# Performance work log

Measured on AMD Instinct MI355X. Metric: run time of the kernel, lower is better.

Reference implementation:

```python
import jax, jax.numpy as jnp
from jax import lax
import numpy as np

# hyperparams (from init_kwargs)
NB_CLASSES = 100
SZ_EMBED = 128
SCALE = 3.0
LAM = 0.7          # np.random.beta(1,1) draw, fixed for determinism
OT_EPS = 0.05
SINK_THRESH = 0.1
SINK_MAX_ITER = 100
DN = ('NCHW', 'OIHW', 'NCHW')


def l2norm(x, axis):
    # F.normalize: x / max(||x||, 1e-12)
    n = jnp.sqrt(jnp.sum(x * x, axis=axis, keepdims=True))
    return x / jnp.maximum(n, 1e-12)


def encode(x, W_enc, W_feat):
    c = jax.nn.relu(lax.conv_general_dilated(x, W_enc, (2, 2), 'SAME', dimension_numbers=DN))
    f = jax.nn.relu(lax.conv_general_dilated(c, W_feat, (1, 1), 'SAME', dimension_numbers=DN))
    feat = f.mean(axis=(2, 3))  # (B, SZ_EMBED)
    return c, feat


def decode(c, W_dec):
    return lax.conv_transpose(c, W_dec, (2, 2), 'SAME', dimension_numbers=DN)


def sinkhorn(K, u, v):
    # faithful to torch loop: update r, c; break when mean|r-r0| < thresh
    def cond(s):
        i, r, c, err = s
        return jnp.logical_and(i < SINK_MAX_ITER, err >= SINK_THRESH)

    def body(s):
        i, r, c, _ = s
        r0 = r
        r = u / jnp.einsum('bij,bj->bi', K, c)
        c = v / jnp.einsum('bji,bj->bi', K, r)
        err = jnp.mean(jnp.abs(r - r0))
        return (i + 1, r, c, err)

    init = (jnp.int32(0), jnp.ones_like(u), jnp.ones_like(v), jnp.array(jnp.inf, K.dtype))
    _, r, c, _ = lax.while_loop(cond, body, init)
    return r[:, :, None] * c[:, None, :] * K  # (B, S, S)


def pair_wise_wdist(x, y):
    B, C, H, W = x.shape
    S = H * W
    xf = l2norm(x.reshape(B, C, S), axis=1)  # unit vectors per spatial location
    yf = l2norm(y.reshape(B, C, S), axis=1)
    sim = jnp.einsum('bcs,bcm->bsm', xf, yf)  # (B, S, S)
    # ||x-y||^2 = 2 - 2*sim for unit vectors (avoids (B,C,S,S) intermediate)
    dist1 = jnp.sqrt(jnp.maximum(2.0 - 2.0 * sim, 0.0) + 1e-6)
    u = jnp.full((B, S), 1.0 / S, dtype=sim.dtype)
    v = jnp.full((B, S), 1.0 / S, dtype=sim.dtype)
    K = lax.stop_gradient(jnp.exp(-(1.0 - sim) / OT_EPS))  # torch.no_grad
    T = lax.stop_gradient(sinkhorn(K, u, v))
    dist = jnp.sum(T * dist1, axis=(1, 2))
    return dist, T


def metric_loss(X, labels, P):
    Pn = SCALE * l2norm(P, axis=-1)
    Xn = SCALE * l2norm(X, axis=-1)
    # squared pairwise distance X vs P
    D = (jnp.sum(Xn * Xn, -1)[:, None] + jnp.sum(Pn * Pn, -1)[None, :]
         - 2.0 * Xn @ Pn.T)
    logp = jax.nn.log_softmax(-D, axis=-1)
    # smoothing_const=0 -> one-hot labels
    return -jnp.mean(logp[jnp.arange(X.shape[0]), labels])


def reference(xa, xb, la, lb, proxies, W_enc, W_feat, W_dec):
    B, C, H, W = xa.shape
    c_xa, feat_xa = encode(xa, W_enc, W_feat)
    xa_hat = decode(c_xa, W_dec)
    c_xb, feat_xb = encode(xb, W_enc, W_feat)
    xb_hat = decode(c_xb, W_dec)

    struct_dist, T = pair_wise_wdist(xa, xb)

    xa_fl = l2norm(xa, axis=1).reshape(B, C, -1)
    xb_fl = l2norm(xb, axis=1).reshape(B, C, -1)
    # faithful to the original einsum (k and j summed independently)
    xb_tomix = jnp.einsum('bmk,bji->bmi', xa_fl, T)
    xa_tomix = jnp.einsum('bmk,bji->bmi', xb_fl, jnp.swapaxes(T, 1, 2))

    lam = LAM
    mixed_xa = (lam * xa.reshape(B, C, -1) + (1 - lam) * xa_tomix).reshape(B, C, H, W)
    mixed_xb = (lam * xb.reshape(B, C, -1) + (1 - lam) * xb_tomix).reshape(B, C, H, W)

    l_x_rec_a = jnp.mean(jnp.square(xa_hat - xa))
    l_x_rec_b = jnp.mean(jnp.square(xb_hat - xb))

    feat_ma = mixed_xa.mean(axis=(2, 3))  # adaptive_avg_pool2d -> (B, C)
    feat_mb = mixed_xb.mean(axis=(2, 3))

    l_c_rec_a = metric_loss(feat_xa, la, proxies)
    l_c_rec_b = metric_loss(feat_xb, lb, proxies)
    l_c_rec_ma = lam * metric_loss(feat_ma, la, proxies) + (1 - lam) * metric_loss(feat_ma, lb, proxies)
    l_c_rec_mb = lam * metric_loss(feat_mb, lb, proxies) + (1 - lam) * metric_loss(feat_mb, la, proxies)

    l_total = l_x_rec_a + l_x_rec_b + l_c_rec_a + l_c_rec_b + l_c_rec_ma + l_c_rec_mb
    return jnp.stack([l_total, l_x_rec_a, l_x_rec_b, l_c_rec_a, l_c_rec_b, l_c_rec_ma, l_c_rec_mb])


def setup_inputs() -> dict:
    key = jax.random.key(0)
    ks = jax.random.split(key, 8)
    B, C, H, W = 32, 128, 32, 32
    xa = jax.random.normal(ks[0], (B, C, H, W), jnp.float32)
    xb = jax.random.normal(ks[1], (B, C, H, W), jnp.float32)
    la = jax.random.randint(ks[2], (B,), 0, NB_CLASSES)
    lb = jax.random.randint(ks[3], (B,), 0, NB_CLASSES)
    proxies = jax.random.normal(ks[4], (NB_CLASSES, SZ_EMBED), jnp.float32) / 8.0
    W_enc = jax.random.normal(ks[5], (2 * C, C, 3, 3), jnp.float32) * 0.02
    W_feat = jax.random.normal(ks[6], (SZ_EMBED, 2 * C, 3, 3), jnp.float32) * 0.02
    W_dec = jax.random.normal(ks[7], (C, 2 * C, 3, 3), jnp.float32) * 0.02
    return {"xa": xa, "xb": xb, "la": la, "lb": lb, "proxies": proxies,
            "W_enc": W_enc, "W_feat": W_feat, "W_dec": W_dec}
```

## Files before the change

### kernel.cpp

```cpp
#include <hip/hip_runtime.h>
#include <hip/hip_bf16.h>

#define DEVI __device__ __forceinline__

constexpr int B_ = 32, CI = 128, CM = 256, H_ = 32, W_ = 32;
constexpr int S_ = 1024, NB = 100;
constexpr float LAMF = 0.7f, ILAMF = 0.3f, SCALEF = 3.0f;
constexpr size_t XSZ = (size_t)32 * 16 * 1156 * 8;
constexpr size_t XBS = (size_t)16 * 1156 * 8;
constexpr size_t CSZ = (size_t)32 * 32 * 324 * 8;
constexpr size_t CBS = (size_t)32 * 324 * 8;

typedef short bf8 __attribute__((ext_vector_type(8)));
typedef float f4 __attribute__((ext_vector_type(4)));
typedef unsigned short u16;
typedef unsigned int u32;

struct alignas(8) us4 { u16 v[4]; };
struct alignas(16) us8 { u16 v[8]; };

__device__ __constant__ int TAPD9c[9] = {0, 2, 6, 8, 1, 7, 3, 5, 4};

DEVI u16 f2bf(float f) {
    unsigned u = __builtin_bit_cast(unsigned, f);
    u += 0x7FFFu + ((u >> 16) & 1u);
    return (u16)(u >> 16);
}
DEVI float bf2f(u16 h) {
    unsigned u = ((unsigned)h) << 16;
    return __builtin_bit_cast(float, u);
}

DEVI void gll16(const void* g, void* l) {
    __builtin_amdgcn_global_load_lds(
        (const __attribute__((address_space(1))) u32*)g,
        (__attribute__((address_space(3))) u32*)l, 16, 0, 0);
}

DEVI float waveSum(float v) {
#pragma unroll
    for (int off = 32; off > 0; off >>= 1) v += __shfl_down(v, off, 64);
    return v;
}
DEVI float blockSum256(float v, float* lds4) {
    v = waveSum(v);
    int wid = threadIdx.x >> 6, lane = threadIdx.x & 63;
    __syncthreads();
    if (lane == 0) lds4[wid] = v;
    __syncthreads();
    return lds4[0] + lds4[1] + lds4[2] + lds4[3];
}
DEVI float blockSum128(float v, float* lds2) {
    v = waveSum(v);
    int wid = threadIdx.x >> 6, lane = threadIdx.x & 63;
    __syncthreads();
    if (lane == 0) lds2[wid] = v;
    __syncthreads();
    return lds2[0] + lds2[1];
}
DEVI float blockMax128(float v, float* lds2) {
#pragma unroll
    for (int off = 32; off > 0; off >>= 1) v = fmaxf(v, __shfl_down(v, off, 64));
    int wid = threadIdx.x >> 6, lane = threadIdx.x & 63;
    __syncthreads();
    if (lane == 0) lds2[wid] = v;
    __syncthreads();
    return fmaxf(lds2[0], lds2[1]);
}

__global__ __launch_bounds__(256) void k_prep_w(const float* __restrict__ We,
                                                const float* __restrict__ Wf,
                                                const float* __restrict__ Wd,
                                                u16* __restrict__ A1p,
                                                u16* __restrict__ A2p,
                                                u16* __restrict__ A3p) {
    int i = blockIdx.x * 256 + threadIdx.x;
    {
        int e = i & 7, s = (i >> 3) & 511, j = i >> 12;
        int Mt = j / 36, kc = j - Mt * 36;
        int tap = kc >> 2, cq = kc & 3;
        int q = s >> 7, m = s & 127;
        int oc = Mt * 128 + m, ch = cq * 32 + q * 8 + e;
        A1p[i] = f2bf(We[((size_t)oc * CI + ch) * 9 + tap]);
    }
    {
        int e = i & 7, s = (i >> 3) & 511, kc = i >> 12;
        int tapi = kc >> 3, cq = kc & 7;
        int q = s >> 7, m = s & 127;
        int ch = cq * 32 + q * 8 + e;
        A2p[i] = f2bf(Wf[((size_t)m * CM + ch) * 9 + tapi]);
        A3p[i] = f2bf(Wd[((size_t)m * CM + ch) * 9 + TAPD9c[tapi]]);
    }
}

__global__ __launch_bounds__(128) void k_prox(const float* __restrict__ P,
                                              float* __restrict__ PnT,
                                              float* __restrict__ pn2) {
    __shared__ float lds2[2];
    int k = blockIdx.x, t = threadIdx.x;
    float v = P[k * CI + t];
    float ss = blockSum128(v * v, lds2);
    float sc = SCALEF / fmaxf(sqrtf(ss), 1e-12f);
    float pv = v * sc;
    PnT[t * NB + k] = pv;
    float s2 = blockSum128(pv * pv, lds2);
    if (t == 0) pn2[k] = s2;
}

__global__ __launch_bounds__(256) void k_ring(u16* __restrict__ xpad, u16* __restrict__ cpad) {
    int b = blockIdx.x, ab = blockIdx.y, t = threadIdx.x;
    u16* xp = xpad + (size_t)ab * XSZ + (size_t)b * XBS;
    u16* cp = cpad + (size_t)ab * CSZ + (size_t)b * CBS;
    us8 z = {};
    for (int i = t; i < 132 * 16; i += 256) {
        int cc = i / 132, rp = i - cc * 132;
        int pos;
        if (rp < 68) pos = (rp < 34) ? (32 * 34 + rp) : (33 * 34 + rp - 34);
        else { int r2 = rp - 68; pos = (r2 >> 1) * 34 + 32 + (r2 & 1); }
        *(us8*)(xp + ((size_t)cc * 1156 + pos) * 8) = z;
    }
    for (int i = t; i < 68 * 32; i += 256) {
        int cc = i / 68, rp = i - cc * 68;
        int pos;
        if (rp < 36) pos = (rp < 18) ? rp : (17 * 18 + rp - 18);
        else { int r2 = rp - 36; pos = (1 + (r2 >> 1)) * 18 + ((r2 & 1) ? 17 : 0); }
        *(us8*)(cp + ((size_t)cc * 324 + pos) * 8) = z;
    }
}

__global__ __launch_bounds__(256) void k_xpose(const float* __restrict__ xa,
                                               const float* __restrict__ xb,
                                               u16* __restrict__ xpad,
                                               float* __restrict__ meanbuf) {
    __shared__ float ldsx[128][64];
    __shared__ float sred[256];
    __shared__ float sinv[64];
    int b = blockIdx.x, yg = blockIdx.y, ab = blockIdx.z;
    int t = threadIdx.x;
    const float* x = (ab ? xb : xa) + (size_t)b * CI * S_ + yg * 64;
    int c4 = t >> 6, p = t & 63;
    for (int c0 = 0; c0 < 32; ++c0) {
        int c = c0 * 4 + c4;
        ldsx[c][p] = x[(size_t)c * S_ + p];
    }
    __syncthreads();
    int qc = t >> 6;
    int y = yg * 2 + (p >> 5), xcol = p & 31;
    u16* ox = xpad + (size_t)ab * XSZ + (size_t)b * XBS;
    float ss = 0.f;
#pragma unroll
    for (int c8 = 0; c8 < 4; ++c8) {
        int cb = qc * 32 + c8 * 8;
        int cc = cb >> 3;
        us8 pk;
#pragma unroll
        for (int j = 0; j < 8; ++j) {
            float v = ldsx[cb + j][p];
            ss = fmaf(v, v, ss);
            pk.v[j] = f2bf(v);
        }
        *(us8*)(ox + ((size_t)cc * 1156 + y * 34 + xcol) * 8) = pk;
    }
    sred[t] = ss;
    __syncthreads();
    if (t < 64) {
        float s = sred[t] + sred[t + 64] + sred[t + 128] + sred[t + 192];
        sinv[t] = 1.f / fmaxf(sqrtf(s), 1e-12f);
    }
    __syncthreads();
    int c = t >> 1, h = t & 1;
    float sx = 0.f, sf = 0.f;
    for (int i = 0; i < 32; ++i) {
        int p2 = h * 32 + ((i + c) & 31);
        float v = ldsx[c][p2];
        sx += v;
        sf = fmaf(v, sinv[p2], sf);
    }
    sx += __shfl_xor(sx, 1, 64);
    sf += __shfl_xor(sf, 1, 64);
    if (!(t & 1)) {
        atomicAdd(&meanbuf[(size_t)ab * 4096 + b * 128 + c], sx * (1.f / 1024.f));
        atomicAdd(&meanbuf[8192 + (size_t)ab * 4096 + b * 128 + c], sf * (1.f / 1024.f));
    }
}

__global__ __launch_bounds__(256, 2) void k_conv1g(const u16* __restrict__ XC,
                                                   const u16* __restrict__ A1p,
                                                   u16* __restrict__ CC) {
    __shared__ u16 sA[2][8192];
    __shared__ u16 sB[2][4096];
    int t = threadIdx.x, l = t & 63, l15 = l & 15, lq = l >> 4, w = t >> 6;
    int wm = w & 1, wn = w >> 1;
    int Nt = blockIdx.x, b = blockIdx.y;
    int ab = blockIdx.z & 1, Mt = blockIdx.z >> 1;
    const u16* xc = XC + (size_t)ab * XSZ + (size_t)b * XBS;
    const u16* Ag = A1p + (size_t)Mt * (36 * 4096);
    int bpos0 = (8 * Nt + 2 * (l >> 4)) * 34 + 2 * (l & 15);
    const int po1[9] = {0, 1, 2, 34, 35, 36, 68, 69, 70};

    auto stageA = [&](int buf, int kcA) {
        const u16* ga = Ag + (size_t)kcA * 4096 + t * 8;
        u16* da = &sA[buf][w * 512];
#pragma unroll
        for (int i = 0; i < 4; ++i) gll16(ga + i * 2048, da + i * 2048);
    };
    auto stageB = [&](int buf, int po, int s) {
#pragma unroll
        for (int i = 0; i < 2; ++i) {
            int ks = i * 4 + w;
            gll16(xc + ((size_t)(s * 8 + ks) * 1156 + bpos0 + po) * 8,
                  &sB[buf][(size_t)ks * 512]);
        }
    };

    f4 acc[4][2] = {};
    stageA(0, 0);
    stageB(0, 0, 0);
    int cur = 0;
#pragma unroll
    for (int ti = 0; ti < 9; ++ti) {
        const int po = po1[ti];
        const int poN = (ti < 8) ? po1[ti + 1] : 0;
#pragma unroll 1
        for (int s = 0; s < 2; ++s) {
            __syncthreads();
            bool last = (ti == 8) && (s == 1);
            if (!last) {
                int tin = (s < 1) ? ti : ti + 1;
                int sn = (s < 1) ? 1 : 0;
                stageA(cur ^ 1, tin * 4 + sn * 2);
                stageB(cur ^ 1, (s < 1) ? po : poN, sn);
            }
            const u16* As = sA[cur];
            const u16* Bs = sB[cur];
#pragma unroll
            for (int kc2 = 0; kc2 < 2; ++kc2) {
                bf8 af[4], bv[2];
#pragma unroll
                for (int mf = 0; mf < 4; ++mf)
                    af[mf] = *(const bf8*)(As + ((kc2 * 4 + lq) * 128 + wm * 64 + mf * 16 + l15) * 8);
#pragma unroll
                for (int nf = 0; nf < 2; ++nf)
                    bv[nf] = *(const bf8*)(Bs + ((kc2 * 4 + lq) * 64 + wn * 32 + nf * 16 + l15) * 8);
#pragma unroll
                for (int mf = 0; mf < 4; ++mf)
#pragma unroll
                    for (int nf = 0; nf < 2; ++nf)
                        acc[mf][nf] = __builtin_amdgcn_mfma_f32_16x16x32_bf16(af[mf], bv[nf], acc[mf][nf], 0, 0, 0);
            }
            cur ^= 1;
        }
    }
    u16* cb = CC + (size_t)ab * CSZ + (size_t)b * CBS;
#pragma unroll
    for (int mf = 0; mf < 4; ++mf) {
        int mc = Mt * 128 + wm * 64 + mf * 16 + lq * 4;
#pragma unroll
        for (int nf = 0; nf < 2; ++nf) {
            int nl = wn * 32 + nf * 16 + l15;
            int oh = Nt * 4 + (nl >> 4), ow = nl & 15;
            int posO = (1 + oh) * 18 + 1 + ow;
            us4 pk;
#pragma unroll
            for (int r = 0; r < 4; ++r) pk.v[r] = f2bf(fmaxf(acc[mf][nf][r], 0.f));
            *(us4*)(cb + ((size_t)(mc >> 3) * 324 + posO) * 8 + (mc & 7)) = pk;
        }
    }
}


#define KSTEP(ACC, SUBV, KYV, KXV, HN, KCAN)                                        \
    {                                                                               \
        __syncthreads();                                                            \
        if (HN) stageA(cur ^ 1, (KCAN));                                            \
        const u16* As = sA[cur];                                                    \
        _Pragma("unroll") for (int kc2 = 0; kc2 < 2; ++kc2) {                       \
            bf8 af[4], bv[4];                                                       \
            _Pragma("unroll") for (int mf = 0; mf < 4; ++mf)                        \
                af[mf] = *(const bf8*)(As + kc2 * 4096 + aq + mf * 128);            \
            _Pragma("unroll") for (int nf = 0; nf < 4; ++nf)                        \
                bv[nf] = *(const bf8*)(sS + ((2 * (SUBV) + kc2) * 720 + bq +        \
                                             (nf + (KYV)) * 18 + (KXV)) * 8);      \
            _Pragma("unroll") for (int mf = 0; mf < 4; ++mf)                        \
                _Pragma("unroll") for (int nf = 0; nf < 4; ++nf)                    \
                    ACC[mf][nf] = __builtin_amdgcn_mfma_f32_16x16x32_bf16(          \
                        af[mf], bv[nf], ACC[mf][nf], 0, 0, 0);                      \
        }                                                                           \
        cur ^= 1;                                                                   \
    }

#define FLUSH(ACC, PY, PX)                                                          \
    _Pragma("unroll") for (int mf = 0; mf < 4; ++mf) {                              \
        int mc = wm * 64 + mf * 16 + lq * 4;                                        \
        const u16* xrow = xq + (size_t)(mc >> 3) * 1156 * 8 + (mc & 7);             \
        _Pragma("unroll") for (int nf = 0; nf < 4; ++nf) {                          \
            int n = wn * 64 + nf * 16 + l15;                                        \
            int oh = 8 * Nt + (n >> 4), ow = n & 15;                                \
            int Y = 2 * oh + (PY), X = 2 * ow + (PX);                               \
            us4 xv = *(const us4*)(xrow + (size_t)(Y * 34 + X) * 8);                \
            _Pragma("unroll") for (int r = 0; r < 4; ++r) {                         \
                float d = ACC[mf][nf][r] - bf2f(xv.v[r]);                           \
                ss = fmaf(d, d, ss);                                                \
            }                                                                       \
        }                                                                           \
    }

__global__ __launch_bounds__(256, 2) void k_cde7(const u16* __restrict__ CC,
                                                 const u16* __restrict__ A2p,
                                                 const u16* __restrict__ A3p,
                                                 const u16* __restrict__ XC,
                                                 float* __restrict__ feats,
                                                 float* __restrict__ pr) {
    __shared__ u16 sS[23040];
    __shared__ u16 sA[2][8192];
    __shared__ float lds4[4];
    int t = threadIdx.x, l = t & 63, l15 = l & 15, lq = l >> 4, w = t >> 6;
    int wm = w & 1, wn = w >> 1;
    int Nt = blockIdx.x, b = blockIdx.y;
    int ab = blockIdx.z & 1, type = blockIdx.z >> 1;
    const u16* cbb = CC + (size_t)ab * CSZ + (size_t)b * CBS;
    const u16* xq = XC + (size_t)ab * XSZ + (size_t)b * XBS;
    const u16* Ag = type ? A3p : A2p;
    int r0 = 8 * Nt;
    int aq = (lq * 128 + wm * 64 + l15) * 8;
    int bq = lq * 180 + wn * 72 + l15;

    auto stageA = [&](int buf, int kcA) {
        const u16* ga = Ag + (size_t)kcA * 4096 + t * 8;
        u16* da = &sA[buf][w * 512];
#pragma unroll
        for (int i = 0; i < 4; ++i) gll16(ga + i * 2048, da + i * 2048);
    };
    auto stage_slab = [&](int h) {
        if (t < 180) {
#pragma unroll 1
            for (int ccL = 0; ccL < 16; ++ccL) {
                int cc = h * 16 + ccL;
                us8 v = *(const us8*)(cbb + ((size_t)cc * 324 + r0 * 18 + t) * 8);
                *(us8*)(sS + ((size_t)ccL * 180 + t) * 8) = v;
            }
        }
    };

    int cur = 0;
    float ss = 0.f;
    if (type == 0) {
        f4 acc[4][4] = {};
        stage_slab(0);
        stageA(0, 0);
#pragma unroll
        for (int h = 0; h < 2; ++h) {
            if (h == 1) { __syncthreads(); stage_slab(1); }
#pragma unroll 1
            for (int st = 0; st < 18; ++st) {
                int s = h * 18 + st;
                int ti = st >> 1, sub = st & 1;
                int ky = ti / 3, kx = ti - ky * 3;
                bool hn = s < 35;
                int s1 = hn ? s + 1 : 0;
                int h1 = s1 / 18, rr = s1 - h1 * 18;
                int kcan = (rr >> 1) * 8 + h1 * 4 + (rr & 1) * 2;
                KSTEP(acc, sub, ky, kx, hn, kcan);
            }
        }
        float* fo = feats + ((size_t)ab * B_ + b) * CI;
#pragma unroll
        for (int mf = 0; mf < 4; ++mf)
#pragma unroll
            for (int r = 0; r < 4; ++r) {
                float v = 0.f;
#pragma unroll
                for (int nf = 0; nf < 4; ++nf) v += fmaxf(acc[mf][nf][r], 0.f);
                v += __shfl_xor(v, 1, 64);
                v += __shfl_xor(v, 2, 64);
                v += __shfl_xor(v, 4, 64);
                v += __shfl_xor(v, 8, 64);
                if (l15 == 0)
                    atomicAdd(fo + wm * 64 + mf * 16 + lq * 4 + r, v * (1.f / 256.f));
            }
    } else if (type == 1) {
        f4 accP[4][4] = {}, accQ[4][4] = {};
        stage_slab(0);
        stageA(0, 0);
#pragma unroll
        for (int h = 0; h < 2; ++h) {
            if (h == 1) { __syncthreads(); stage_slab(1); }
#pragma unroll 1
            for (int st = 0; st < 8; ++st) {
                int s = h * 10 + st;
                int ip = st >> 1, sub = st & 1;
                int dy = ip >> 1, dx = ip & 1;
                bool hn = s < 19;
                int s1 = hn ? s + 1 : 0;
                int h1 = s1 / 10, rr = s1 - h1 * 10;
                int tapi1 = (rr < 8) ? (rr >> 1) : 8;
                int sub1 = (rr < 8) ? (rr & 1) : (rr - 8);
                int kcan = tapi1 * 8 + h1 * 4 + sub1 * 2;
                KSTEP(accP, sub, dy, dx, hn, kcan);
            }
#pragma unroll 1
            for (int st = 0; st < 2; ++st) {
                int s = h * 10 + 8 + st;
                int sub = st;
                bool hn = s < 19;
                int s1 = hn ? s + 1 : 0;
                int h1 = s1 / 10, rr = s1 - h1 * 10;
                int tapi1 = (rr < 8) ? (rr >> 1) : 8;
                int sub1 = (rr < 8) ? (rr & 1) : (rr - 8);
                int kcan = tapi1 * 8 + h1 * 4 + sub1 * 2;
                KSTEP(accQ, sub, 1, 1, hn, kcan);
            }
        }
        FLUSH(accP, 0, 0);
        FLUSH(accQ, 1, 1);
        ss = blockSum256(ss, lds4);
        if (t == 0) atomicAdd(pr + ab, ss);
    } else {
        f4 accP[4][4] = {}, accQ[4][4] = {};
        stage_slab(0);
        stageA(0, 32);
#pragma unroll
        for (int h = 0; h < 2; ++h) {
            if (h == 1) { __syncthreads(); stage_slab(1); }
#pragma unroll 1
            for (int st = 0; st < 4; ++st) {
                int s = h * 8 + st;
                int ip = st >> 1, sub = st & 1;
                bool hn = s < 15;
                int s1 = hn ? s + 1 : 0;
                int h1 = s1 >> 3, rr = s1 & 7;
                int kcan = (4 + (rr >> 1)) * 8 + h1 * 4 + (rr & 1) * 2;
                KSTEP(accP, sub, ip, 1, hn, kcan);
            }
#pragma unroll 1
            for (int st = 0; st < 4; ++st) {
                int s = h * 8 + 4 + st;
                int iq = st >> 1, sub = st & 1;
                bool hn = s < 15;
                int s1 = hn ? s + 1 : 0;
                int h1 = s1 >> 3, rr = s1 & 7;
                int kcan = (4 + (rr >> 1)) * 8 + h1 * 4 + (rr & 1) * 2;
                KSTEP(accQ, sub, 1, iq, hn, kcan);
            }
        }
        FLUSH(accP, 0, 1);
        FLUSH(accQ, 1, 0);
        ss = blockSum256(ss, lds4);
        if (t == 0) atomicAdd(pr + ab, ss);
    }
}

#undef KSTEP
#undef FLUSH

__global__ __launch_bounds__(128) void k_metric(const float* __restrict__ feats,
                                                const float* __restrict__ meanbuf,
                                                const float* __restrict__ PnT,
                                                const float* __restrict__ pn2,
                                                const int* __restrict__ la,
                                                const int* __restrict__ lb,
                                                float* __restrict__ mo) {
    __shared__ float lds2[2];
    __shared__ float xs[128];
    int blk = blockIdx.x;
    int t = threadIdx.x;
    int b = blk & 31;
    float xv;
    if (blk < 64) xv = feats[(size_t)blk * CI + t];
    else if (blk < 96) xv = LAMF * meanbuf[b * 128 + t] + ILAMF * meanbuf[12288 + b * 128 + t];
    else xv = LAMF * meanbuf[4096 + b * 128 + t] + ILAMF * meanbuf[8192 + b * 128 + t];
    float ssq = blockSum128(xv * xv, lds2);
    float sc = SCALEF / fmaxf(sqrtf(ssq), 1e-12f);
    float xn = xv * sc;
    xs[t] = xn;
    float xn2 = blockSum128(xn * xn, lds2);
    bool active = (t < NB);
    float Dk = 1e30f;
    if (active) {
        float dot = 0.f;
#pragma unroll 8
        for (int e = 0; e < CI; ++e) dot = fmaf(xs[e], PnT[e * NB + t], dot);
        Dk = xn2 + pn2[t] - 2.f * dot;
    }
    float z = active ? -Dk : -1e30f;
    float m = blockMax128(z, lds2);
    float e = active ? expf(z - m) : 0.f;
    float se = blockSum128(e, lds2);
    float lse = m + logf(se);
    if (t == 0) mo[blk * 3 + 0] = lse;
    int A = la[b], Bb = lb[b];
    if (t == A) mo[blk * 3 + 1] = Dk;
    if (t == Bb) mo[blk * 3 + 2] = Dk;
}

__global__ __launch_bounds__(128) void k_final(const float* __restrict__ pr,
                                               const float* __restrict__ mo,
                                               float* __restrict__ out) {
    __shared__ float mla[4], mlb[4];
    int t = threadIdx.x;
    const float* m = mo + t * 3;
    float ula = m[0] + m[1];
    float ulb = m[0] + m[2];
#pragma unroll
    for (int off = 16; off > 0; off >>= 1) {
        ula += __shfl_down(ula, off, 32);
        ulb += __shfl_down(ulb, off, 32);
    }
    if ((t & 31) == 0) { mla[t >> 5] = ula * (1.f / 32.f); mlb[t >> 5] = ulb * (1.f / 32.f); }
    __syncthreads();
    if (t == 0) {
        float lxa = pr[0] * (1.f / 4194304.f);
        float lxb = pr[1] * (1.f / 4194304.f);
        float lca = mla[0];
        float lcb = mlb[1];
        float lcma = LAMF * mla[2] + ILAMF * mlb[2];
        float lcmb = LAMF * mlb[3] + ILAMF * mla[3];
        out[0] = lxa + lxb + lca + lcb + lcma + lcmb;
        out[1] = lxa; out[2] = lxb; out[3] = lca; out[4] = lcb; out[5] = lcma; out[6] = lcmb;
    }
}

extern "C" void kernel_launch(void* const* d_in, const int* in_sizes, int n_in,
                              void* d_out, int out_size, void* d_ws, size_t ws_size,
                              hipStream_t stream) {
    const float* xa = (const float*)d_in[0];
    const float* xb = (const float*)d_in[1];
    const int* la = (const int*)d_in[2];
    const int* lb = (const int*)d_in[3];
    const float* P = (const float*)d_in[4];
    const float* We = (const float*)d_in[5];
    const float* Wf = (const float*)d_in[6];
    const float* Wd = (const float*)d_in[7];

    char* w = (char*)d_ws;
    const size_t XPAD_B = XSZ * 2 * sizeof(u16);
    const size_t CPAD_B = CSZ * 2 * sizeof(u16);
    const size_t AW_B = (size_t)294912 * 2;
    u16* xpad = (u16*)w;                 w += XPAD_B;
    u16* cpad = (u16*)w;                 w += CPAD_B;
    u16* A1p = (u16*)w;                  w += AW_B;
    u16* A2p = (u16*)w;                  w += AW_B;
    u16* A3p = (u16*)w;                  w += AW_B;
    float* PnT = (float*)w;              w += 12800 * 4;
    float* pn2 = (float*)w;              w += 128 * 4;
    float* feats = (float*)w;            w += 8192 * 4;
    float* meanbuf = (float*)w;          w += 16384 * 4;
    float* pr = (float*)w;               w += 16 * 4;
    float* mo = (float*)w;               w += 384 * 4;
    float* out = (float*)d_out;

    hipMemsetAsync(feats, 0, (8192 + 16384 + 16) * sizeof(float), stream);

    k_prep_w<<<1152, 256, 0, stream>>>(We, Wf, Wd, A1p, A2p, A3p);
    k_prox<<<NB, 128, 0, stream>>>(P, PnT, pn2);
    k_ring<<<dim3(32, 2), 256, 0, stream>>>(xpad, cpad);
    k_xpose<<<dim3(32, 16, 2), 256, 0, stream>>>(xa, xb, xpad, meanbuf);
    k_conv1g<<<dim3(4, 32, 4), 256, 0, stream>>>(xpad, A1p, cpad);
    k_cde7<<<dim3(2, 32, 6), 256, 0, stream>>>(cpad, A2p, A3p, xpad, feats, pr);
    k_metric<<<128, 128, 0, stream>>>(feats, meanbuf, PnT, pn2, la, lb, mo);
    k_final<<<1, 128, 0, stream>>>(pr, mo, out);
}
```

Measured before the change: 104.3 us.

## Triple-buffer weight staging in fused conv kernel with explicit vmcnt waits

The weight-tile staging in the fused feature/decoder conv kernel moves from a double buffer with one barrier per step to a three-slot ring prefetched two steps ahead. Each step now waits on the async global-to-LDS loads with explicit s_waitcnt vmcnt counts before a raw s_barrier, rather than a full __syncthreads. The goal is to hide more global-load latency behind the MFMA work. The cost is 16 KB more LDS per block, which may reduce occupancy at two blocks per CU, and reliance on hand-counted outstanding loads that the slab staging could disturb.

```diff
diff --git a/kernel.cpp b/kernel.cpp
--- a/kernel.cpp
+++ b/kernel.cpp
@@ -269,50 +269,54 @@
 }
 
 
-#define KSTEP(ACC, SUBV, KYV, KXV, HN, KCAN)                                        \
-    {                                                                               \
-        __syncthreads();                                                            \
-        if (HN) stageA(cur ^ 1, (KCAN));                                            \
-        const u16* As = sA[cur];                                                    \
-        _Pragma("unroll") for (int kc2 = 0; kc2 < 2; ++kc2) {                       \
-            bf8 af[4], bv[4];                                                       \
-            _Pragma("unroll") for (int mf = 0; mf < 4; ++mf)                        \
-                af[mf] = *(const bf8*)(As + kc2 * 4096 + aq + mf * 128);            \
-            _Pragma("unroll") for (int nf = 0; nf < 4; ++nf)                        \
-                bv[nf] = *(const bf8*)(sS + ((2 * (SUBV) + kc2) * 720 + bq +        \
-                                             (nf + (KYV)) * 18 + (KXV)) * 8);      \
-            _Pragma("unroll") for (int mf = 0; mf < 4; ++mf)                        \
-                _Pragma("unroll") for (int nf = 0; nf < 4; ++nf)                    \
-                    ACC[mf][nf] = __builtin_amdgcn_mfma_f32_16x16x32_bf16(          \
-                        af[mf], bv[nf], ACC[mf][nf], 0, 0, 0);                      \
-        }                                                                           \
-        cur ^= 1;                                                                   \
-    }
-
-#define FLUSH(ACC, PY, PX)                                                          \
-    _Pragma("unroll") for (int mf = 0; mf < 4; ++mf) {                              \
-        int mc = wm * 64 + mf * 16 + lq * 4;                                        \
-        const u16* xrow = xq + (size_t)(mc >> 3) * 1156 * 8 + (mc & 7);             \
-        _Pragma("unroll") for (int nf = 0; nf < 4; ++nf) {                          \
-            int n = wn * 64 + nf * 16 + l15;                                        \
-            int oh = 8 * Nt + (n >> 4), ow = n & 15;                                \
-            int Y = 2 * oh + (PY), X = 2 * ow + (PX);                               \
-            us4 xv = *(const us4*)(xrow + (size_t)(Y * 34 + X) * 8);                \
-            _Pragma("unroll") for (int r = 0; r < 4; ++r) {                         \
-                float d = ACC[mf][nf][r] - bf2f(xv.v[r]);                           \
-                ss = fmaf(d, d, ss);                                                \
-            }                                                                       \
-        }                                                                           \
-    }
-
-__global__ __launch_bounds__(256, 2) void k_cde7(const u16* __restrict__ CC,
+#define COMPUTE(ACC)                                                           \
+    {                                                                          \
+        const u16* As = sA + ib3 * 8192;                                       \
+        _Pragma("unroll") for (int kc2 = 0; kc2 < 2; ++kc2) {                  \
+            bf8 af[4], bv[4];                                                  \
+            _Pragma("unroll") for (int mf = 0; mf < 4; ++mf)                   \
+                af[mf] = *(const bf8*)(As + kc2 * 4096 + aq + mf * 128);       \
+            _Pragma("unroll") for (int nf = 0; nf < 4; ++nf)                   \
+                bv[nf] = *(const bf8*)(sS + ((2 * sub + kc2) * 720 + bq +      \
+                                             (nf + oy) * 18 + ox) * 8);        \
+            _Pragma("unroll") for (int mf = 0; mf < 4; ++mf)                   \
+                _Pragma("unroll") for (int nf = 0; nf < 4; ++nf)               \
+                    ACC[mf][nf] = __builtin_amdgcn_mfma_f32_16x16x32_bf16(     \
+                        af[mf], bv[nf], ACC[mf][nf], 0, 0, 0);                 \
+        }                                                                      \
+    }
+
+#define PIPE_SYNC(NSTEP)                                                       \
+    if (s + 2 < (NSTEP)) asm volatile("s_waitcnt vmcnt(8)" ::: "memory");      \
+    else if (s + 1 < (NSTEP)) asm volatile("s_waitcnt vmcnt(4)" ::: "memory"); \
+    else asm volatile("s_waitcnt vmcnt(0)" ::: "memory");                      \
+    __builtin_amdgcn_s_barrier();                                              \
+    __builtin_amdgcn_sched_barrier(0);
+
+#define FLUSH(ACC, PY, PX)                                                     \
+    _Pragma("unroll") for (int mf = 0; mf < 4; ++mf) {                         \
+        int mc = wm * 64 + mf * 16 + lq * 4;                                   \
+        const u16* xrow = xq + (size_t)(mc >> 3) * 1156 * 8 + (mc & 7);        \
+        _Pragma("unroll") for (int nf = 0; nf < 4; ++nf) {                     \
+            int n = wn * 64 + nf * 16 + l15;                                   \
+            int oh = 8 * Nt + (n >> 4), ow = n & 15;                           \
+            int Y = 2 * oh + (PY), X = 2 * ow + (PX);                          \
+            us4 xv = *(const us4*)(xrow + (size_t)(Y * 34 + X) * 8);           \
+            _Pragma("unroll") for (int r = 0; r < 4; ++r) {                    \
+                float d = ACC[mf][nf][r] - bf2f(xv.v[r]);                      \
+                ss = fmaf(d, d, ss);                                           \
+            }                                                                  \
+        }                                                                      \
+    }
+
+__global__ __launch_bounds__(256, 2) void k_cde8(const u16* __restrict__ CC,
                                                  const u16* __restrict__ A2p,
                                                  const u16* __restrict__ A3p,
                                                  const u16* __restrict__ XC,
                                                  float* __restrict__ feats,
                                                  float* __restrict__ pr) {
     __shared__ u16 sS[23040];
-    __shared__ u16 sA[2][8192];
+    __shared__ u16 sA[3 * 8192];
     __shared__ float lds4[4];
     int t = threadIdx.x, l = t & 63, l15 = l & 15, lq = l >> 4, w = t >> 6;
     int wm = w & 1, wn = w >> 1;
@@ -327,7 +331,7 @@
 
     auto stageA = [&](int buf, int kcA) {
         const u16* ga = Ag + (size_t)kcA * 4096 + t * 8;
-        u16* da = &sA[buf][w * 512];
+        u16* da = &sA[buf * 8192 + w * 512];
 #pragma unroll
         for (int i = 0; i < 4; ++i) gll16(ga + i * 2048, da + i * 2048);
     };
@@ -342,26 +346,26 @@
         }
     };
 
-    int cur = 0;
     float ss = 0.f;
     if (type == 0) {
         f4 acc[4][4] = {};
+        stageA(0, 0);
+        stageA(1, 2);
         stage_slab(0);
-        stageA(0, 0);
-#pragma unroll
-        for (int h = 0; h < 2; ++h) {
-            if (h == 1) { __syncthreads(); stage_slab(1); }
+        __syncthreads();
 #pragma unroll 1
-            for (int st = 0; st < 18; ++st) {
-                int s = h * 18 + st;
-                int ti = st >> 1, sub = st & 1;
-                int ky = ti / 3, kx = ti - ky * 3;
-                bool hn = s < 35;
-                int s1 = hn ? s + 1 : 0;
-                int h1 = s1 / 18, rr = s1 - h1 * 18;
-                int kcan = (rr >> 1) * 8 + h1 * 4 + (rr & 1) * 2;
-                KSTEP(acc, sub, ky, kx, hn, kcan);
-            }
+        for (int s = 0; s < 36; ++s) {
+            if (s == 18) { __syncthreads(); stage_slab(1); __syncthreads(); }
+            if (s + 2 < 36) {
+                int s2 = s + 2, h2 = s2 / 18, rr2 = s2 - h2 * 18;
+                stageA(s2 % 3, (rr2 >> 1) * 8 + h2 * 4 + (rr2 & 1) * 2);
+            }
+            PIPE_SYNC(36);
+            int ib3 = s % 3;
+            int rr = (s < 18) ? s : s - 18;
+            int sub = rr & 1, ti = rr >> 1;
+            int oy = ti / 3, ox = ti - oy * 3;
+            COMPUTE(acc);
         }
         float* fo = feats + ((size_t)ab * B_ + b) * CI;
 #pragma unroll
@@ -380,35 +384,29 @@
             }
     } else if (type == 1) {
         f4 accP[4][4] = {}, accQ[4][4] = {};
+        stageA(0, 0);
+        stageA(1, 2);
         stage_slab(0);
-        stageA(0, 0);
-#pragma unroll
-        for (int h = 0; h < 2; ++h) {
-            if (h == 1) { __syncthreads(); stage_slab(1); }
+        __syncthreads();
 #pragma unroll 1
-            for (int st = 0; st < 8; ++st) {
-                int s = h * 10 + st;
-                int ip = st >> 1, sub = st & 1;
-                int dy = ip >> 1, dx = ip & 1;
-                bool hn = s < 19;
-                int s1 = hn ? s + 1 : 0;
-                int h1 = s1 / 10, rr = s1 - h1 * 10;
-                int tapi1 = (rr < 8) ? (rr >> 1) : 8;
-                int sub1 = (rr < 8) ? (rr & 1) : (rr - 8);
-                int kcan = tapi1 * 8 + h1 * 4 + sub1 * 2;
-                KSTEP(accP, sub, dy, dx, hn, kcan);
-            }
-#pragma unroll 1
-            for (int st = 0; st < 2; ++st) {
-                int s = h * 10 + 8 + st;
-                int sub = st;
-                bool hn = s < 19;
-                int s1 = hn ? s + 1 : 0;
-                int h1 = s1 / 10, rr = s1 - h1 * 10;
-                int tapi1 = (rr < 8) ? (rr >> 1) : 8;
-                int sub1 = (rr < 8) ? (rr & 1) : (rr - 8);
-                int kcan = tapi1 * 8 + h1 * 4 + sub1 * 2;
-                KSTEP(accQ, sub, 1, 1, hn, kcan);
+        for (int s = 0; s < 20; ++s) {
+            if (s == 10) { __syncthreads(); stage_slab(1); __syncthreads(); }
+            if (s + 2 < 20) {
+                int s2 = s + 2, h2 = s2 / 10, rr2 = s2 - h2 * 10;
+                int tapi2 = (rr2 < 8) ? (rr2 >> 1) : 8;
+                int sub2 = (rr2 < 8) ? (rr2 & 1) : (rr2 - 8);
+                stageA(s2 % 3, tapi2 * 8 + h2 * 4 + sub2 * 2);
+            }
+            PIPE_SYNC(20);
+            int ib3 = s % 3;
+            int rr = (s < 10) ? s : s - 10;
+            if (rr < 8) {
+                int sub = rr & 1, tp = rr >> 1;
+                int oy = tp >> 1, ox = tp & 1;
+                COMPUTE(accP);
+            } else {
+                int sub = rr - 8, oy = 1, ox = 1;
+                COMPUTE(accQ);
             }
         }
         FLUSH(accP, 0, 0);
@@ -417,30 +415,26 @@
         if (t == 0) atomicAdd(pr + ab, ss);
     } else {
         f4 accP[4][4] = {}, accQ[4][4] = {};
+        stageA(0, 32);
+        stageA(1, 34);
         stage_slab(0);
-        stageA(0, 32);
-#pragma unroll
-        for (int h = 0; h < 2; ++h) {
-            if (h == 1) { __syncthreads(); stage_slab(1); }
+        __syncthreads();
 #pragma unroll 1
-            for (int st = 0; st < 4; ++st) {
-                int s = h * 8 + st;
-                int ip = st >> 1, sub = st & 1;
-                bool hn = s < 15;
-                int s1 = hn ? s + 1 : 0;
-                int h1 = s1 >> 3, rr = s1 & 7;
-                int kcan = (4 + (rr >> 1)) * 8 + h1 * 4 + (rr & 1) * 2;
-                KSTEP(accP, sub, ip, 1, hn, kcan);
-            }
-#pragma unroll 1
-            for (int st = 0; st < 4; ++st) {
-                int s = h * 8 + 4 + st;
-                int iq = st >> 1, sub = st & 1;
-                bool hn = s < 15;
-                int s1 = hn ? s + 1 : 0;
-                int h1 = s1 >> 3, rr = s1 & 7;
-                int kcan = (4 + (rr >> 1)) * 8 + h1 * 4 + (rr & 1) * 2;
-                KSTEP(accQ, sub, 1, iq, hn, kcan);
+        for (int s = 0; s < 16; ++s) {
+            if (s == 8) { __syncthreads(); stage_slab(1); __syncthreads(); }
+            if (s + 2 < 16) {
+                int s2 = s + 2, h2 = s2 >> 3, rr2 = s2 & 7;
+                stageA(s2 % 3, (4 + (rr2 >> 1)) * 8 + h2 * 4 + (rr2 & 1) * 2);
+            }
+            PIPE_SYNC(16);
+            int ib3 = s % 3;
+            int rr = s & 7;
+            if (rr < 4) {
+                int sub = rr & 1, oy = rr >> 1, ox = 1;
+                COMPUTE(accP);
+            } else {
+                int sub = rr & 1, oy = 1, ox = (rr >> 1) - 2;
+                COMPUTE(accQ);
             }
         }
         FLUSH(accP, 0, 1);
@@ -450,7 +444,8 @@
     }
 }
 
-#undef KSTEP
+#undef COMPUTE
+#undef PIPE_SYNC
 #undef FLUSH
 
 __global__ __launch_bounds__(128) void k_metric(const float* __restrict__ feats,
@@ -556,7 +551,7 @@
     k_ring<<<dim3(32, 2), 256, 0, stream>>>(xpad, cpad);
     k_xpose<<<dim3(32, 16, 2), 256, 0, stream>>>(xa, xb, xpad, meanbuf);
     k_conv1g<<<dim3(4, 32, 4), 256, 0, stream>>>(xpad, A1p, cpad);
-    k_cde7<<<dim3(2, 32, 6), 256, 0, stream>>>(cpad, A2p, A3p, xpad, feats, pr);
+    k_cde8<<<dim3(2, 32, 6), 256, 0, stream>>>(cpad, A2p, A3p, xpad, feats, pr);
     k_metric<<<128, 128, 0, stream>>>(feats, meanbuf, PnT, pn2, la, lb, mo);
     k_final<<<1, 128, 0, stream>>>(pr, mo, out);
 }
```

Measured after the change: 120.3 us. +15.3%, slower.
